# Optimization experiments

Measured on AMD Instinct MI355X. Metric: run time of the kernel, lower is better.

## Reference

```python
import jax, jax.numpy as jnp
import numpy as np

B, S, HID = 2, 2048, 2048
NK, NV, DK, DV, K = 16, 32, 128, 128, 4
KEY_DIM = NK * DK          # 2048
VAL_DIM = NV * DV          # 4096
CONV_DIM = 2 * KEY_DIM + VAL_DIM  # 8192
EPS = 1e-6


def setup_inputs() -> dict:
    key = jax.random.key(0)
    ks = jax.random.split(key, 8)
    n = lambda k, shape, sc: jax.random.normal(k, shape, jnp.float32) * sc
    return {
        "hidden_states": n(ks[0], (B, S, HID), 1.0),
        "W_qkv": n(ks[1], (CONV_DIM, HID), 0.02),
        "W_z": n(ks[2], (VAL_DIM, HID), 0.02),
        "W_b": n(ks[3], (NV, HID), 0.02),
        "W_a": n(ks[4], (NV, HID), 0.02),
        "conv_w": n(ks[5], (CONV_DIM, K), 0.3),   # depthwise conv weight, squeeze(1) of [C,1,K]
        "norm_w": jnp.ones((DV,), jnp.float32),
        "W_out": n(ks[6], (HID, VAL_DIM), 0.02),
        "dt_bias": jnp.ones((NV,), jnp.float32),
        "A_log": jnp.zeros((NV,), jnp.float32),
    }


def _l2norm(t):
    return t * jax.lax.rsqrt(jnp.sum(t * t, axis=-1, keepdims=True) + EPS)


def _forward(hidden_states, W_qkv, W_z, W_b, W_a, conv_w, norm_w, W_out, dt_bias, A_log):
    b_, s_, _ = hidden_states.shape
    mixed = hidden_states @ W_qkv.T                     # [B,S,CONV_DIM]
    z = (hidden_states @ W_z.T).reshape(b_, s_, NV, DV)  # gate branch
    b_proj = hidden_states @ W_b.T                      # [B,S,NV]
    a_proj = hidden_states @ W_a.T                      # [B,S,NV]

    # causal depthwise conv1d (groups=CONV_DIM, no bias) + silu
    x = jnp.transpose(mixed, (0, 2, 1))                 # [B,C,S]
    x = jnp.pad(x, ((0, 0), (0, 0), (K - 1, 0)))
    x = jax.lax.conv_general_dilated(
        x, conv_w[:, None, :], window_strides=(1,), padding="VALID",
        feature_group_count=CONV_DIM)
    mixed = jnp.transpose(jax.nn.silu(x), (0, 2, 1))    # [B,S,CONV_DIM]

    q, k, v = jnp.split(mixed, [KEY_DIM, 2 * KEY_DIM], axis=-1)
    q = q.reshape(b_, s_, NK, DK)
    k = k.reshape(b_, s_, NK, DK)
    v = v.reshape(b_, s_, NV, DV)

    beta = jax.nn.sigmoid(b_proj)                                    # [B,S,NV]
    g = -jnp.exp(A_log) * jax.nn.softplus(a_proj + dt_bias)          # [B,S,NV], log decay

    rep = NV // NK
    q = jnp.repeat(q, rep, axis=2)                      # GQA expand -> [B,S,NV,DK]
    k = jnp.repeat(k, rep, axis=2)
    q = _l2norm(q)
    k = _l2norm(k)
    scale = DK ** -0.5

    def step(state, inp):  # state: [B,NV,DK,DV]
        qt, kt, vt, gt, bt = inp  # [B,NV,DK],[B,NV,DK],[B,NV,DV],[B,NV],[B,NV]
        state = state * jnp.exp(gt)[..., None, None]
        mem = jnp.einsum('bhk,bhkv->bhv', kt, state)
        delta = (vt - mem) * bt[..., None]
        state = state + jnp.einsum('bhk,bhv->bhkv', kt, delta)
        ot = jnp.einsum('bhk,bhkv->bhv', qt * scale, state)
        return state, ot

    init = jnp.zeros((b_, NV, DK, DV), jnp.float32)
    xs = (jnp.moveaxis(q, 1, 0), jnp.moveaxis(k, 1, 0), jnp.moveaxis(v, 1, 0),
          jnp.moveaxis(g, 1, 0), jnp.moveaxis(beta, 1, 0))
    _, o = jax.lax.scan(step, init, xs)                 # [S,B,NV,DV]
    o = jnp.moveaxis(o, 0, 1)                           # [B,S,NV,DV]

    # RMSNormGated over head_v_dim, then silu(z) gate
    var = jnp.mean(o * o, axis=-1, keepdims=True)
    o = o * jax.lax.rsqrt(var + EPS) * norm_w
    o = (o * jax.nn.silu(z)).reshape(b_, s_, VAL_DIM)
    return o @ W_out.T


def reference(hidden_states, W_qkv, W_z, W_b, W_a, conv_w, norm_w, W_out, dt_bias, A_log):
    return _forward(hidden_states, W_qkv, W_z, W_b, W_a, conv_w, norm_w, W_out, dt_bias, A_log)
```

## Files before the change

### kernel.cpp

```cpp
#include <hip/hip_runtime.h>
#include <hip/hip_bf16.h>
#include <math.h>

#define DEVI __device__ __forceinline__

typedef __attribute__((ext_vector_type(4))) float f32x4;
typedef __attribute__((ext_vector_type(8))) short s16x8;
typedef __attribute__((ext_vector_type(4))) unsigned int u32x4;

DEVI float bf2f(ushort u){ union{unsigned int i; float f;} x; x.i = ((unsigned int)u)<<16; return x.f; }
DEVI ushort f2bf(float f){ union{float f; unsigned int i;} x; x.f = f;
  unsigned int r = x.i + 0x7fffu + ((x.i>>16)&1u); return (ushort)(r>>16); }

#define MFMA16(a,b,c) __builtin_amdgcn_mfma_f32_16x16x32_bf16(a,b,c,0,0,0)

__global__ __launch_bounds__(256) void cvt_bf16(const float* __restrict__ in, ushort* __restrict__ out){
  int i = blockIdx.x*256 + threadIdx.x;
  float4 v = ((const float4*)in)[i];
  ushort4 o; o.x = f2bf(v.x); o.y = f2bf(v.y); o.z = f2bf(v.z); o.w = f2bf(v.w);
  ((ushort4*)out)[i] = o;
}

DEVI void gl_lds16(const ushort* g, ushort* l){
  __builtin_amdgcn_global_load_lds((const __attribute__((address_space(1))) void*)g,
                                   (__attribute__((address_space(3))) void*)l, 16, 0, 0);
}

#define SBAR() __builtin_amdgcn_s_barrier()
#define LGKM0() do{ asm volatile("s_waitcnt lgkmcnt(0)" ::: "memory"); __builtin_amdgcn_sched_barrier(0); }while(0)
#define VMC6() asm volatile("s_waitcnt vmcnt(6)" ::: "memory")

template<int BF16_OUT>
__global__ __launch_bounds__(512, 2) void gemm256(const ushort* __restrict__ A,
                                                  const ushort* __restrict__ B,
                                                  void* __restrict__ Cv,
                                                  int M, int N, int K){
  __shared__ ushort smem[65536];
  __shared__ ushort dummy[4096];
  const int tid = threadIdx.x, w = tid>>6, lane = tid&63;
  const int fr = lane&15, quad = lane>>4;
  const int wm = w>>2, wn = w&3;
  const int NT = K>>6;

  const int nwg = gridDim.x, bid = blockIdx.x;
  const int wg = (bid&7)*(nwg>>3) + (bid>>3);
  const int nbn = N>>8;
  const long tileM = (long)(wg/nbn)<<8, tileN = (long)(wg%nbn)<<8;

  const int rr  = (tid&63)>>2;
  const int cc  = ((tid&3)*8) ^ ((rr&8)?16:0);
  const int row0 = (w>>1)*16 + rr;
  const int col0 = (w&1)*32 + cc;
  const long off0 = (long)row0*K + col0;
  const long h64 = 64l*K;

  const ushort* pA0 = A + tileM*K + off0;
  const ushort* pA1 = pA0 + 128l*K;
  const ushort* pB0 = B + tileN*K + off0;
  const ushort* pB1 = pB0 + 128l*K;

  const int dw = w*512;
  ushort* dmy = dummy + dw;

#define ST_A0(bb,tt) do{ if((tt)<NT){ const long kk=(long)(tt)<<6; \
    gl_lds16(pA0+kk, smem+(bb)*32768+dw);        gl_lds16(pA1+kk, smem+(bb)*32768+8192+dw);} \
    else { gl_lds16(pA0, dmy); gl_lds16(pA1, dmy);} }while(0)
#define ST_A1(bb,tt) do{ if((tt)<NT){ const long kk=((long)(tt)<<6)+h64; \
    gl_lds16(pA0+kk, smem+(bb)*32768+4096+dw);   gl_lds16(pA1+kk, smem+(bb)*32768+12288+dw);} \
    else { gl_lds16(pA0, dmy); gl_lds16(pA1, dmy);} }while(0)
#define ST_B0(bb,tt) do{ if((tt)<NT){ const long kk=(long)(tt)<<6; \
    gl_lds16(pB0+kk, smem+(bb)*32768+16384+dw);  gl_lds16(pB1+kk, smem+(bb)*32768+24576+dw);} \
    else { gl_lds16(pB0, dmy); gl_lds16(pB1, dmy);} }while(0)
#define ST_B1(bb,tt) do{ if((tt)<NT){ const long kk=((long)(tt)<<6)+h64; \
    gl_lds16(pB0+kk, smem+(bb)*32768+20480+dw);  gl_lds16(pB1+kk, smem+(bb)*32768+28672+dw);} \
    else { gl_lds16(pB0, dmy); gl_lds16(pB1, dmy);} }while(0)

  const int baseF = fr*32 + ((quad*8) ^ ((fr&8)?16:0));
  const int sB = (wn&1)*4;

  f32x4 acc[8][4];
  #pragma unroll
  for (int i=0;i<8;i++)
    #pragma unroll
    for (int j=0;j<4;j++) acc[i][j] = (f32x4){0.f,0.f,0.f,0.f};

  ST_A0(0,0); ST_B0(0,0); ST_B1(0,0); ST_A1(0,0);
  ST_A0(1,1); ST_B0(1,1); ST_B1(1,1);
  VMC6();
  SBAR();

  #pragma unroll 2
  for (int t=0; t<NT; ++t){
    const int bs = t&1;
    const ushort* SA = smem + bs*32768 + wm*8192;
    const ushort* SB = smem + bs*32768 + 16384 + (wn>>1)*8192;
    s16x8 af[4][2], bl[2][2], bh[2][2];
    #pragma unroll
    for (int mt=0;mt<4;mt++)
      #pragma unroll
      for (int ks=0;ks<2;ks++)
        af[mt][ks] = *(const s16x8*)(SA + ((mt*2+ks)<<9) + baseF);
    #pragma unroll
    for (int nt=0;nt<2;nt++)
      #pragma unroll
      for (int ks=0;ks<2;ks++)
        bl[nt][ks] = *(const s16x8*)(SB + (((sB+nt)*2+ks)<<9) + baseF);
    ST_A1(bs^1, t+1);
    SBAR(); LGKM0();
    __builtin_amdgcn_s_setprio(1);
    #pragma unroll
    for (int mt=0;mt<4;mt++)
      #pragma unroll
      for (int nt=0;nt<2;nt++){
        acc[mt][nt] = MFMA16(af[mt][0], bl[nt][0], acc[mt][nt]);
        acc[mt][nt] = MFMA16(af[mt][1], bl[nt][1], acc[mt][nt]);
      }
    __builtin_amdgcn_s_setprio(0);
    SBAR();
    #pragma unroll
    for (int nt=0;nt<2;nt++)
      #pragma unroll
      for (int ks=0;ks<2;ks++)
        bh[nt][ks] = *(const s16x8*)(SB + (((sB+2+nt)*2+ks)<<9) + baseF);
    ST_A0(bs, t+2);
    SBAR(); LGKM0();
    __builtin_amdgcn_s_setprio(1);
    #pragma unroll
    for (int mt=0;mt<4;mt++)
      #pragma unroll
      for (int nt=0;nt<2;nt++){
        acc[mt][2+nt] = MFMA16(af[mt][0], bh[nt][0], acc[mt][2+nt]);
        acc[mt][2+nt] = MFMA16(af[mt][1], bh[nt][1], acc[mt][2+nt]);
      }
    __builtin_amdgcn_s_setprio(0);
    SBAR();
    #pragma unroll
    for (int mt=0;mt<4;mt++)
      #pragma unroll
      for (int ks=0;ks<2;ks++)
        af[mt][ks] = *(const s16x8*)(SA + (((4+mt)*2+ks)<<9) + baseF);
    ST_B0(bs, t+2);
    SBAR(); LGKM0();
    __builtin_amdgcn_s_setprio(1);
    #pragma unroll
    for (int mt=0;mt<4;mt++)
      #pragma unroll
      for (int nt=0;nt<2;nt++){
        acc[4+mt][nt] = MFMA16(af[mt][0], bl[nt][0], acc[4+mt][nt]);
        acc[4+mt][nt] = MFMA16(af[mt][1], bl[nt][1], acc[4+mt][nt]);
      }
    __builtin_amdgcn_s_setprio(0);
    SBAR();
    ST_B1(bs, t+2);
    SBAR();
    __builtin_amdgcn_s_setprio(1);
    #pragma unroll
    for (int mt=0;mt<4;mt++)
      #pragma unroll
      for (int nt=0;nt<2;nt++){
        acc[4+mt][2+nt] = MFMA16(af[mt][0], bh[nt][0], acc[4+mt][2+nt]);
        acc[4+mt][2+nt] = MFMA16(af[mt][1], bh[nt][1], acc[4+mt][2+nt]);
      }
    __builtin_amdgcn_s_setprio(0);
    VMC6();
    SBAR();
  }
#undef ST_A0
#undef ST_A1
#undef ST_B0
#undef ST_B1

  const long Rb = tileM + wm*128 + quad*4;
  const long Cb = tileN + wn*64 + fr;
  if (BF16_OUT){
    ushort* C = (ushort*)Cv;
    #pragma unroll
    for (int mt=0;mt<8;mt++)
      #pragma unroll
      for (int r=0;r<4;r++){
        const long row = Rb + mt*16 + r;
        #pragma unroll
        for (int nt=0;nt<4;nt++)
          C[row*(long)N + Cb + nt*16] = f2bf(acc[mt][nt][r]);
      }
  } else {
    float* C = (float*)Cv;
    #pragma unroll
    for (int mt=0;mt<8;mt++)
      #pragma unroll
      for (int r=0;r<4;r++){
        const long row = Rb + mt*16 + r;
        #pragma unroll
        for (int nt=0;nt<4;nt++)
          C[row*(long)N + Cb + nt*16] = acc[mt][nt][r];
      }
  }
}

template<int BF16_OUT>
__global__ __launch_bounds__(256, 2) void gemm_bt(const ushort* __restrict__ A,
                                                  const ushort* __restrict__ B,
                                                  void* __restrict__ Cv,
                                                  int M, int N, int K){
  __shared__ ushort As[128*32];
  __shared__ ushort Bs[128*32];
  const int nb = N >> 7;
  const int tile_m = (blockIdx.x / nb) << 7;
  const int tile_n = (blockIdx.x % nb) << 7;
  const int tid  = threadIdx.x;
  const int w    = tid >> 6;
  const int lane = tid & 63;

  const int ca = w*2;
  const long rowA = tile_m + ca*16 + (lane>>2);
  const long rowB = tile_n + ca*16 + (lane>>2);
  const int  colE = (lane&3)*8;
  const ushort* pA0 = A + rowA*(long)K + colE;
  const ushort* pA1 = pA0 + 16l*K;
  const ushort* pB0 = B + rowB*(long)K + colE;
  const ushort* pB1 = pB0 + 16l*K;
  ushort* lA0 = As + ca*512;
  ushort* lA1 = As + ca*512 + 512;
  ushort* lB0 = Bs + ca*512;
  ushort* lB1 = Bs + ca*512 + 512;

  const int wr = (w>>1)<<6;
  const int wc = (w&1)<<6;
  const int fr = lane & 15;
  const int fk = (lane>>4)<<3;

  f32x4 acc[4][4];
  #pragma unroll
  for (int i=0;i<4;i++)
    #pragma unroll
    for (int j=0;j<4;j++) acc[i][j] = (f32x4){0.f,0.f,0.f,0.f};

  for (int k0 = 0; k0 < K; k0 += 32){
    __syncthreads();
    gl_lds16(pA0, lA0);
    gl_lds16(pA1, lA1);
    gl_lds16(pB0, lB0);
    gl_lds16(pB1, lB1);
    __syncthreads();
    s16x8 af[4], bfr[4];
    #pragma unroll
    for (int t=0;t<4;t++){
      af[t]  = *(const s16x8*)(As + (wr + t*16 + fr)*32 + fk);
      bfr[t] = *(const s16x8*)(Bs + (wc + t*16 + fr)*32 + fk);
    }
    #pragma unroll
    for (int mt=0;mt<4;mt++)
      #pragma unroll
      for (int nt=0;nt<4;nt++)
        acc[mt][nt] = MFMA16(af[mt], bfr[nt], acc[mt][nt]);
    pA0 += 32; pA1 += 32; pB0 += 32; pB1 += 32;
  }

  const int crow = tile_m + wr + ((lane>>4)<<2);
  const int ccol = tile_n + wc + (lane&15);
  if (BF16_OUT){
    ushort* C = (ushort*)Cv;
    #pragma unroll
    for (int mt=0;mt<4;mt++)
      #pragma unroll
      for (int r=0;r<4;r++){
        long row = crow + mt*16 + r;
        #pragma unroll
        for (int nt=0;nt<4;nt++)
          C[row*(long)N + ccol + nt*16] = f2bf(acc[mt][nt][r]);
      }
  } else {
    float* C = (float*)Cv;
    #pragma unroll
    for (int mt=0;mt<4;mt++)
      #pragma unroll
      for (int r=0;r<4;r++){
        long row = crow + mt*16 + r;
        #pragma unroll
        for (int nt=0;nt<4;nt++)
          C[row*(long)N + ccol + nt*16] = acc[mt][nt][r];
      }
  }
}

__global__ __launch_bounds__(256) void ba_post(const float* __restrict__ bapr,
    const float* __restrict__ dtb, const float* __restrict__ alog,
    float* __restrict__ beta, float* __restrict__ glog){
  const int idx = blockIdx.x*256 + threadIdx.x;
  const int m = idx >> 6, j = idx & 63;
  const float v = bapr[(long)m*128 + j];
  if (j < 32){
    beta[(long)m*32 + j] = 1.f/(1.f+expf(-v));
  } else {
    const int n = j - 32;
    float ap = v + dtb[n];
    float sp = (ap > 20.f) ? ap : log1pf(expf(ap));
    glog[(long)m*32 + n] = -expf(alog[n]) * sp;
  }
}

__global__ __launch_bounds__(256) void conv_qkv2(const ushort* __restrict__ mixed,
    const float* __restrict__ convw, ushort* __restrict__ qn, ushort* __restrict__ kn,
    ushort* __restrict__ vv){
  const long m0 = (long)blockIdx.x * 32;
  const int ct = blockIdx.y;
  const int ch = (ct<<11) + threadIdx.x*8;
  const ushort* base = mixed + ch;

  ushort* outp; int mode; float qsc = 1.f;
  if (ct == 0){ outp = qn + ch;        mode = 0; qsc = 0.08838834764831845f; }
  else if (ct == 1){ outp = kn + (ch-2048); mode = 1; }
  else { outp = vv + (ch-4096); mode = 2; }

  float cw0[8], cw1[8], cw2[8], cw3[8];
  #pragma unroll
  for (int e=0;e<8;e++){
    float4 wv = *(const float4*)(convw + (long)(ch+e)*4);
    cw0[e]=wv.x; cw1[e]=wv.y; cw2[e]=wv.z; cw3[e]=wv.w;
  }

#define LDROW(PTR, R) do{ s16x8 _v = *(const s16x8*)(PTR); \
    _Pragma("unroll") \
    for (int e=0;e<8;e++) R[e] = bf2f((ushort)_v[e]); }while(0)

#define STEP(P0,P1,P2,P3,MR) do{ \
    float y[8]; float ss = 0.f; \
    _Pragma("unroll") \
    for (int e=0;e<8;e++){ \
      float a = P0[e]*cw0[e]; \
      a += P1[e]*cw1[e]; \
      a += P2[e]*cw2[e]; \
      a += P3[e]*cw3[e]; \
      float sv = a / (1.f + expf(-a)); \
      y[e] = sv; ss += sv*sv; } \
    if (mode < 2){ \
      ss += __shfl_xor(ss,1); ss += __shfl_xor(ss,2); \
      ss += __shfl_xor(ss,4); ss += __shfl_xor(ss,8); \
      const float r_ = rsqrtf(ss + 1e-6f) * qsc; \
      s16x8 ov; \
      _Pragma("unroll") \
      for (int e=0;e<8;e++) ov[e] = (short)f2bf(y[e]*r_); \
      *(s16x8*)(outp + (MR)*2048) = ov; \
    } else { \
      s16x8 ov; \
      _Pragma("unroll") \
      for (int e=0;e<8;e++) ov[e] = (short)f2bf(y[e]); \
      *(s16x8*)(outp + (MR)*4096) = ov; \
    } \
  }while(0)

  float w3[8], w2[8], w1[8];
  if (((int)m0 & 2047) == 0){
    #pragma unroll
    for (int e=0;e<8;e++){ w3[e]=0.f; w2[e]=0.f; w1[e]=0.f; }
  } else {
    LDROW(base + (m0-3)*8192, w3);
    LDROW(base + (m0-2)*8192, w2);
    LDROW(base + (m0-1)*8192, w1);
  }

  long m = m0;
  for (int it=0; it<8; ++it){
    float r0[8], r1[8], r2[8], r3[8];
    LDROW(base + (m+0)*8192, r0);
    LDROW(base + (m+1)*8192, r1);
    LDROW(base + (m+2)*8192, r2);
    LDROW(base + (m+3)*8192, r3);
    STEP(w3,w2,w1,r0, m+0);
    STEP(w2,w1,r0,r1, m+1);
    STEP(w1,r0,r1,r2, m+2);
    STEP(r0,r1,r2,r3, m+3);
    #pragma unroll
    for (int e=0;e<8;e++){ w3[e]=r1[e]; w2[e]=r2[e]; w1[e]=r3[e]; }
    m += 4;
  }
#undef LDROW
#undef STEP
}

__global__ __launch_bounds__(256) void chunk_prep(
    const ushort* __restrict__ qn, const ushort* __restrict__ kn,
    const float* __restrict__ beta, const float* __restrict__ glog,
    ushort* __restrict__ Tg, ushort* __restrict__ Mg, float* __restrict__ cumLgG){
  const int bid = blockIdx.x;
  const int bh = bid >> 6, ch = bid & 63;
  const int b = bh>>5, h = bh&31, hq = h>>1;
  const long tch = (long)b*2048 + ch*32;
  const int tid = threadIdx.x, w = tid>>6, lane = tid&63;
  const int quad = lane>>4, l15 = lane&15;

  __shared__ __attribute__((aligned(16))) ushort Kl[32][136];
  __shared__ __attribute__((aligned(16))) ushort Ql[32][136];
  __shared__ float Asl[32][33];
  __shared__ float Lgl[32], Btl[32];

  const int sc = tid>>3, ss = (tid&7)*16;
  {
    const ushort* kp = kn + (tch+sc)*2048 + hq*128 + ss;
    const ushort* qp = qn + (tch+sc)*2048 + hq*128 + ss;
    *(u32x4*)&Kl[sc][ss] = *(const u32x4*)kp; *(u32x4*)&Kl[sc][ss+8] = *(const u32x4*)(kp+8);
    *(u32x4*)&Ql[sc][ss] = *(const u32x4*)qp; *(u32x4*)&Ql[sc][ss+8] = *(const u32x4*)(qp+8);
  }
  if (tid < 64){
    const int c = lane & 31;
    float gv = glog[(tch + c)*32 + h];
    float bv = beta[(tch + c)*32 + h];
    #pragma unroll
    for (int off=1; off<32; off<<=1){
      float t = __shfl_up(gv, off);
      if ((lane & 31) >= off) gv += t;
    }
    if (lane < 32){ Lgl[c] = gv; Btl[c] = bv; cumLgG[(long)bid*32 + c] = gv; }
  }
  __syncthreads();

  const int mt = w>>1, nt = w&1;
  s16x8 ka[4], qa[4], kb[4];
  #pragma unroll
  for (int ks=0; ks<4; ks++){
    ka[ks] = *(const s16x8*)&Kl[mt*16+l15][ks*32 + quad*8];
    qa[ks] = *(const s16x8*)&Ql[mt*16+l15][ks*32 + quad*8];
    kb[ks] = *(const s16x8*)&Kl[nt*16+l15][ks*32 + quad*8];
  }
  f32x4 accK = (f32x4){0.f,0.f,0.f,0.f}, accQ = (f32x4){0.f,0.f,0.f,0.f};
  #pragma unroll
  for (int ks=0; ks<4; ks++){
    accK = MFMA16(ka[ks], kb[ks], accK);
    accQ = MFMA16(qa[ks], kb[ks], accQ);
  }
  const int j = nt*16 + l15;
  const float Lgj = Lgl[j];
  #pragma unroll
  for (int i=0;i<4;i++){
    const int r = mt*16 + quad*4 + i;
    const float e = expf(Lgl[r]-Lgj);
    Asl[r][j] = (r>j) ? -Btl[r]*e*accK[i] : 0.f;
    Mg[(long)bid*1024 + r*32 + j] = (r>=j) ? f2bf(e*accQ[i]) : (ushort)0;
  }
  __syncthreads();

  if (tid < 32){
    const int jc = tid;
    float tc[32];
    #pragma unroll
    for (int c=0;c<32;c++){
      float acc = (c==jc) ? 1.f : 0.f;
      #pragma unroll
      for (int i2=0;i2<c;i2++) acc = fmaf(Asl[c][i2], tc[i2], acc);
      tc[c] = acc;
      Tg[(long)bid*1024 + c*32 + jc] = f2bf(acc);
    }
  }
}

__global__ __launch_bounds__(256, 2) void chunk_scan3(
    const ushort* __restrict__ qn, const ushort* __restrict__ kn,
    const ushort* __restrict__ vv, const float* __restrict__ beta,
    const float* __restrict__ cumLg, const ushort* __restrict__ Tg,
    const ushort* __restrict__ Mg, float* __restrict__ o){
  const int bh = blockIdx.x & 63, sl = blockIdx.x >> 6;
  const int b = bh>>5, h = bh&31, hq = h>>1;
  const int dv0 = sl<<4;
  const int tid = threadIdx.x, w = tid>>6, lane = tid&63;
  const int quad = lane>>4, l15 = lane&15;
  const int rt = w&1, kq = w>>1;

  __shared__ __attribute__((aligned(16))) ushort STl[16][136];
  __shared__ __attribute__((aligned(16))) ushort B0T[16][40];
  __shared__ __attribute__((aligned(16))) ushort DT[16][40];
  __shared__ float Btf[32], eLgl[32], eDf[32];

  const ushort* pKQ = (kq ? qn : kn) + ((long)b*2048 + rt*16 + l15)*2048 + hq*128 + quad*8;
  const ushort* pKT = kn + ((long)b*2048 + quad*8)*2048 + hq*128 + w*32 + l15;
  const ushort* pV  = vv + ((long)b*2048 + rt*16 + quad*4)*4096 + h*128 + dv0 + l15;
  const ushort* pTM = (kq ? Mg : Tg) + (long)bh*65536 + (rt*16 + l15)*32 + quad*8;
  const long pbBase = (long)bh*2048 + tid;
  const float* betaP = beta + ((long)b*2048 + tid)*32 + h;

  s16x8 cKQ[4], nKQ[4], cK0, cK1, nK0, nK1, cTM, nTM;
  ushort cV0=0,cV1=0,cV2=0,cV3=0, nV0=0,nV1=0,nV2=0,nV3=0;
  float cLg = 0.f, nLg = 0.f, cBt = 0.f, nBt = 0.f;

  f32x4 S0 = (f32x4){0.f,0.f,0.f,0.f}, S1 = (f32x4){0.f,0.f,0.f,0.f};

#define LOADCH(PKQ,PK0,PK1,PV0,PV1,PV2,PV3,PTMv,PLG,PBT,CH) do{ \
    const long co = (long)(CH)*65536; \
    _Pragma("unroll") \
    for (int ks=0; ks<4; ks++) PKQ[ks] = *(const s16x8*)(pKQ + co + ks*32); \
    _Pragma("unroll") \
    for (int e=0; e<8; e++){ \
      PK0[e] = (short)pKT[co + (long)e*2048]; \
      PK1[e] = (short)pKT[co + (long)e*2048 + 16]; } \
    if (kq == 0){ \
      const long vo = (long)(CH)*131072; \
      PV0 = pV[vo]; PV1 = pV[vo+4096]; PV2 = pV[vo+8192]; PV3 = pV[vo+12288]; } \
    PTMv = *(const s16x8*)(pTM + (long)(CH)*1024); \
    if (tid < 32){ PLG = cumLg[pbBase + (long)(CH)*32]; PBT = betaP[(long)(CH)*1024]; } \
  }while(0)

  LOADCH(cKQ, cK0, cK1, cV0,cV1,cV2,cV3, cTM, cLg, cBt, 0);

  for (int ch=0; ch<64; ch++){
    const long tch = (long)b*2048 + ch*32;
    LOADCH(nKQ, nK0, nK1, nV0,nV1,nV2,nV3, nTM, nLg, nBt, (ch<63)?(ch+1):63);
    if (tid < 32){
      float lgC = __shfl(cLg, 31);
      Btf[tid] = cBt;
      eLgl[tid] = expf(cLg);
      eDf[tid]  = expf(lgC - cLg);
    }
    {
      ushort4 p0, p1;
      p0.x=f2bf(S0[0]); p0.y=f2bf(S0[1]); p0.z=f2bf(S0[2]); p0.w=f2bf(S0[3]);
      p1.x=f2bf(S1[0]); p1.y=f2bf(S1[1]); p1.z=f2bf(S1[2]); p1.w=f2bf(S1[3]);
      *(ushort4*)&STl[l15][w*32 + quad*4]      = p0;
      *(ushort4*)&STl[l15][w*32 + 16 + quad*4] = p1;
    }
    __syncthreads();
    f32x4 acc = (f32x4){0.f,0.f,0.f,0.f};
    #pragma unroll
    for (int ks=0; ks<4; ks++){
      s16x8 sb = *(const s16x8*)&STl[l15][ks*32 + quad*8];
      acc = MFMA16(cKQ[ks], sb, acc);
    }
    if (kq == 0){
      const int c0r = rt*16 + quad*4;
      ushort4 pb;
      pb.x = f2bf(Btf[c0r+0]*(bf2f(cV0) - eLgl[c0r+0]*acc[0]));
      pb.y = f2bf(Btf[c0r+1]*(bf2f(cV1) - eLgl[c0r+1]*acc[1]));
      pb.z = f2bf(Btf[c0r+2]*(bf2f(cV2) - eLgl[c0r+2]*acc[2]));
      pb.w = f2bf(Btf[c0r+3]*(bf2f(cV3) - eLgl[c0r+3]*acc[3]));
      *(ushort4*)&B0T[l15][rt*16 + quad*4] = pb;
    } else {
      #pragma unroll
      for (int i=0;i<4;i++) acc[i] *= eLgl[rt*16 + quad*4 + i];
    }
    __syncthreads();
    const float eC = eLgl[31];
    s16x8 kta0, kta1;
    #pragma unroll
    for (int e=0;e<8;e++){
      const float ed = eDf[quad*8 + e];
      kta0[e] = (short)f2bf(bf2f((ushort)cK0[e])*ed);
      kta1[e] = (short)f2bf(bf2f((ushort)cK1[e])*ed);
    }
    if (kq == 0){
      s16x8 a = *(const s16x8*)&B0T[l15][quad*8];
      f32x4 Dt = MFMA16(a, cTM, ((f32x4){0.f,0.f,0.f,0.f}));
      #pragma unroll
      for (int i=0;i<4;i++)
        DT[quad*4+i][rt*16 + l15] = f2bf(Dt[i]);
    }
    __syncthreads();
    s16x8 df = *(const s16x8*)&DT[l15][quad*8];
    if (kq == 1){
      f32x4 O = MFMA16(cTM, df, acc);
      #pragma unroll
      for (int i=0;i<4;i++)
        o[(tch + rt*16 + quad*4 + i)*4096 + h*128 + dv0 + l15] = O[i];
    }
    f32x4 t0, t1;
    #pragma unroll
    for (int i=0;i<4;i++){ t0[i] = S0[i]*eC; t1[i] = S1[i]*eC; }
    S0 = MFMA16(kta0, df, t0);
    S1 = MFMA16(kta1, df, t1);
    #pragma unroll
    for (int ks=0; ks<4; ks++) cKQ[ks] = nKQ[ks];
    cK0 = nK0; cK1 = nK1; cTM = nTM;
    cV0 = nV0; cV1 = nV1; cV2 = nV2; cV3 = nV3;
    cLg = nLg; cBt = nBt;
  }
#undef LOADCH
}

__global__ __launch_bounds__(128) void norm_gate(const float* __restrict__ o,
    const ushort* __restrict__ z, const float* __restrict__ normw,
    ushort* __restrict__ og){
  const long mh = blockIdx.x;
  const int d = threadIdx.x;
  float x = o[mh*128 + d];
  float ss = x*x;
  #pragma unroll
  for (int off=32; off; off>>=1) ss += __shfl_xor(ss, off);
  __shared__ float w2[2];
  if ((d&63)==0) w2[d>>6] = ss;
  __syncthreads();
  float r = rsqrtf((w2[0]+w2[1])*(1.f/128.f) + 1e-6f);
  float zz = bf2f(z[mh*128 + d]);
  float sil = zz / (1.f + expf(-zz));
  og[mh*128 + d] = f2bf(x*r*normw[d]*sil);
}

extern "C" void kernel_launch(void* const* d_in, const int* in_sizes, int n_in,
                              void* d_out, int out_size, void* d_ws, size_t ws_size,
                              hipStream_t stream){
  const float* hs    = (const float*)d_in[0];
  const float* Wqkv  = (const float*)d_in[1];
  const float* Wz    = (const float*)d_in[2];
  const float* Wb    = (const float*)d_in[3];
  const float* Wa    = (const float*)d_in[4];
  const float* convw = (const float*)d_in[5];
  const float* normw = (const float*)d_in[6];
  const float* Wout  = (const float*)d_in[7];
  const float* dtb   = (const float*)d_in[8];
  const float* alog  = (const float*)d_in[9];

  char* ws = (char*)d_ws;
  ushort* hsb   = (ushort*)(ws);
  ushort* wqb   = (ushort*)(ws + (16l<<20));
  ushort* wzb   = (ushort*)(ws + (48l<<20));
  ushort* wob   = (ushort*)(ws + (64l<<20));
  ushort* mixed = (ushort*)(ws + (80l<<20));
  ushort* zb    = (ushort*)(ws + (144l<<20));
  float*  beta  = (float*)(ws + (176l<<20));
  float*  cumLg = (float*)(ws + (176l<<20) + (512l<<10));
  float*  glog  = (float*)(ws + (177l<<20));
  ushort* Tg    = (ushort*)(ws + (178l<<20));
  ushort* Mg    = (ushort*)(ws + (186l<<20));
  ushort* wbab  = (ushort*)(ws + (194l<<20));
  float*  bapr  = (float*)(ws + (195l<<20));
  ushort* kn = hsb;  ushort* qn = wzb;  ushort* vvp = wqb;  ushort* og = wqb;
  float*  o_raw = (float*)mixed;

  cvt_bf16<<<8192,  256, 0, stream>>>(hs,   hsb);
  cvt_bf16<<<16384, 256, 0, stream>>>(Wqkv, wqb);
  cvt_bf16<<<8192,  256, 0, stream>>>(Wz,   wzb);
  cvt_bf16<<<8192,  256, 0, stream>>>(Wout, wob);
  cvt_bf16<<<64,    256, 0, stream>>>(Wb,   wbab);
  cvt_bf16<<<64,    256, 0, stream>>>(Wa,   wbab + 65536);

  gemm256<1><<<512, 512, 0, stream>>>(hsb, wqb, (void*)mixed, 4096, 8192, 2048);
  gemm256<1><<<256, 512, 0, stream>>>(hsb, wzb, (void*)zb,    4096, 4096, 2048);
  gemm_bt<0><<<32*1,  256, 0, stream>>>(hsb, wbab, (void*)bapr, 4096, 128,  2048);
  ba_post<<<1024, 256, 0, stream>>>(bapr, dtb, alog, beta, glog);

  conv_qkv2<<<dim3(128,4), 256, 0, stream>>>(mixed, convw, qn, kn, vvp);
  chunk_prep<<<4096, 256, 0, stream>>>(qn, kn, beta, glog, Tg, Mg, cumLg);
  chunk_scan3<<<512, 256, 0, stream>>>(qn, kn, vvp, beta, cumLg, Tg, Mg, o_raw);
  norm_gate<<<131072, 128, 0, stream>>>(o_raw, zb, normw, og);

  gemm_bt<0><<<32*16, 256, 0, stream>>>(og, wob, d_out, 4096, 2048, 4096);
}
```

Measured before the change: 719.2 us.

## Add XCD-grouped tile mapping and 256x128 pipelined GEMM for output projection

Replaces the gemm256 workgroup-to-tile mapping with a grouping where each XCD handles a contiguous block of row and column tiles, to improve L2 reuse of A and B panels. Adds a new 256x128-tile GEMM variant with the same async global-to-LDS double-buffered MFMA pipeline. It is used for the output projection in place of the simpler 128x128 gemm_bt kernel. The grouping parameters are hard-coded per launch and must divide the tile counts exactly.

```diff
diff --git a/kernel.cpp b/kernel.cpp
--- a/kernel.cpp
+++ b/kernel.cpp
@@ -29,12 +29,14 @@
 #define SBAR() __builtin_amdgcn_s_barrier()
 #define LGKM0() do{ asm volatile("s_waitcnt lgkmcnt(0)" ::: "memory"); __builtin_amdgcn_sched_barrier(0); }while(0)
 #define VMC6() asm volatile("s_waitcnt vmcnt(6)" ::: "memory")
+#define VMC4() asm volatile("s_waitcnt vmcnt(4)" ::: "memory")
 
 template<int BF16_OUT>
 __global__ __launch_bounds__(512, 2) void gemm256(const ushort* __restrict__ A,
                                                   const ushort* __restrict__ B,
                                                   void* __restrict__ Cv,
-                                                  int M, int N, int K){
+                                                  int M, int N, int K,
+                                                  int rpx, int cpx){
   __shared__ ushort smem[65536];
   __shared__ ushort dummy[4096];
   const int tid = threadIdx.x, w = tid>>6, lane = tid&63;
@@ -42,10 +44,14 @@
   const int wm = w>>2, wn = w&3;
   const int NT = K>>6;
 
-  const int nwg = gridDim.x, bid = blockIdx.x;
-  const int wg = (bid&7)*(nwg>>3) + (bid>>3);
   const int nbn = N>>8;
-  const long tileM = (long)(wg/nbn)<<8, tileN = (long)(wg%nbn)<<8;
+  const int bid = blockIdx.x;
+  const int xcd = bid & 7, idx = bid >> 3;
+  const int CGn = nbn / cpx;
+  const int rgrp = xcd / CGn, cgrp = xcd % CGn;
+  const int rloc = idx % rpx, cloc = idx / rpx;
+  const long tileM = (long)(rgrp*rpx + rloc) << 8;
+  const long tileN = (long)(cgrp*cpx + cloc) << 8;
 
   const int rr  = (tid&63)>>2;
   const int cc  = ((tid&3)*8) ^ ((rr&8)?16:0);
@@ -192,6 +198,158 @@
         const long row = Rb + mt*16 + r;
         #pragma unroll
         for (int nt=0;nt<4;nt++)
+          C[row*(long)N + Cb + nt*16] = acc[mt][nt][r];
+      }
+  }
+}
+
+template<int BF16_OUT>
+__global__ __launch_bounds__(512, 2) void gemm256n128(const ushort* __restrict__ A,
+                                                      const ushort* __restrict__ B,
+                                                      void* __restrict__ Cv,
+                                                      int M, int N, int K,
+                                                      int rpx, int cpx){
+  __shared__ ushort smem[49152];
+  __shared__ ushort dummy[4096];
+  const int tid = threadIdx.x, w = tid>>6, lane = tid&63;
+  const int fr = lane&15, quad = lane>>4;
+  const int wm = w>>2, wn = w&3;
+  const int NT = K>>6;
+
+  const int nbn = N>>7;
+  const int bid = blockIdx.x;
+  const int xcd = bid & 7, idx = bid >> 3;
+  const int CGn = nbn / cpx;
+  const int rgrp = xcd / CGn, cgrp = xcd % CGn;
+  const int rloc = idx % rpx, cloc = idx / rpx;
+  const long tileM = (long)(rgrp*rpx + rloc) << 8;
+  const long tileN = (long)(cgrp*cpx + cloc) << 7;
+
+  const int rr  = (tid&63)>>2;
+  const int cc  = ((tid&3)*8) ^ ((rr&8)?16:0);
+  const int row0 = (w>>1)*16 + rr;
+  const int col0 = (w&1)*32 + cc;
+  const long off0 = (long)row0*K + col0;
+  const long h64 = 64l*K;
+
+  const ushort* pA0 = A + tileM*K + off0;
+  const ushort* pA1 = pA0 + 128l*K;
+  const ushort* pB0 = B + tileN*K + off0;
+
+  const int dw = w*512;
+  ushort* dmy = dummy + dw;
+
+#define ST_A0(bb,tt) do{ if((tt)<NT){ const long kk=(long)(tt)<<6; \
+    gl_lds16(pA0+kk, smem+(bb)*24576+dw);        gl_lds16(pA1+kk, smem+(bb)*24576+8192+dw);} \
+    else { gl_lds16(pA0, dmy); gl_lds16(pA1, dmy);} }while(0)
+#define ST_A1(bb,tt) do{ if((tt)<NT){ const long kk=((long)(tt)<<6)+h64; \
+    gl_lds16(pA0+kk, smem+(bb)*24576+4096+dw);   gl_lds16(pA1+kk, smem+(bb)*24576+12288+dw);} \
+    else { gl_lds16(pA0, dmy); gl_lds16(pA1, dmy);} }while(0)
+#define ST_B(bb,tt) do{ if((tt)<NT){ const long kk=(long)(tt)<<6; \
+    gl_lds16(pB0+kk, smem+(bb)*24576+16384+dw);  gl_lds16(pB0+kk+h64, smem+(bb)*24576+20480+dw);} \
+    else { gl_lds16(pB0, dmy); gl_lds16(pB0, dmy);} }while(0)
+
+  const int baseF = fr*32 + ((quad*8) ^ ((fr&8)?16:0));
+
+  f32x4 acc[8][2];
+  #pragma unroll
+  for (int i=0;i<8;i++)
+    #pragma unroll
+    for (int j=0;j<2;j++) acc[i][j] = (f32x4){0.f,0.f,0.f,0.f};
+
+  ST_A0(0,0); ST_B(0,0); ST_A1(0,0);
+  ST_A0(1,1); ST_B(1,1);
+  VMC4();
+  SBAR();
+
+  #pragma unroll 2
+  for (int t=0; t<NT; ++t){
+    const int bs = t&1;
+    const ushort* SA = smem + bs*24576 + wm*8192;
+    const ushort* SB = smem + bs*24576 + 16384;
+    s16x8 af[4][2], bl[2], bh[2];
+    #pragma unroll
+    for (int mt=0;mt<4;mt++)
+      #pragma unroll
+      for (int ks=0;ks<2;ks++)
+        af[mt][ks] = *(const s16x8*)(SA + ((mt*2+ks)<<9) + baseF);
+    #pragma unroll
+    for (int ks=0;ks<2;ks++)
+      bl[ks] = *(const s16x8*)(SB + (((wn*2+0)*2+ks)<<9) + baseF);
+    ST_A1(bs^1, t+1);
+    SBAR(); LGKM0();
+    __builtin_amdgcn_s_setprio(1);
+    #pragma unroll
+    for (int mt=0;mt<4;mt++){
+      acc[mt][0] = MFMA16(af[mt][0], bl[0], acc[mt][0]);
+      acc[mt][0] = MFMA16(af[mt][1], bl[1], acc[mt][0]);
+    }
+    __builtin_amdgcn_s_setprio(0);
+    SBAR();
+    #pragma unroll
+    for (int ks=0;ks<2;ks++)
+      bh[ks] = *(const s16x8*)(SB + (((wn*2+1)*2+ks)<<9) + baseF);
+    ST_A0(bs, t+2);
+    SBAR(); LGKM0();
+    __builtin_amdgcn_s_setprio(1);
+    #pragma unroll
+    for (int mt=0;mt<4;mt++){
+      acc[mt][1] = MFMA16(af[mt][0], bh[0], acc[mt][1]);
+      acc[mt][1] = MFMA16(af[mt][1], bh[1], acc[mt][1]);
+    }
+    __builtin_amdgcn_s_setprio(0);
+    SBAR();
+    #pragma unroll
+    for (int mt=0;mt<4;mt++)
+      #pragma unroll
+      for (int ks=0;ks<2;ks++)
+        af[mt][ks] = *(const s16x8*)(SA + (((4+mt)*2+ks)<<9) + baseF);
+    ST_B(bs, t+2);
+    SBAR(); LGKM0();
+    __builtin_amdgcn_s_setprio(1);
+    #pragma unroll
+    for (int mt=0;mt<4;mt++){
+      acc[4+mt][0] = MFMA16(af[mt][0], bl[0], acc[4+mt][0]);
+      acc[4+mt][0] = MFMA16(af[mt][1], bl[1], acc[4+mt][0]);
+    }
+    __builtin_amdgcn_s_setprio(0);
+    SBAR();
+    __builtin_amdgcn_s_setprio(1);
+    #pragma unroll
+    for (int mt=0;mt<4;mt++){
+      acc[4+mt][1] = MFMA16(af[mt][0], bh[0], acc[4+mt][1]);
+      acc[4+mt][1] = MFMA16(af[mt][1], bh[1], acc[4+mt][1]);
+    }
+    __builtin_amdgcn_s_setprio(0);
+    VMC4();
+    SBAR();
+  }
+#undef ST_A0
+#undef ST_A1
+#undef ST_B
+
+  const long Rb = tileM + wm*128 + quad*4;
+  const long Cb = tileN + wn*32 + fr;
+  if (BF16_OUT){
+    ushort* C = (ushort*)Cv;
+    #pragma unroll
+    for (int mt=0;mt<8;mt++)
+      #pragma unroll
+      for (int r=0;r<4;r++){
+        const long row = Rb + mt*16 + r;
+        #pragma unroll
+        for (int nt=0;nt<2;nt++)
+          C[row*(long)N + Cb + nt*16] = f2bf(acc[mt][nt][r]);
+      }
+  } else {
+    float* C = (float*)Cv;
+    #pragma unroll
+    for (int mt=0;mt<8;mt++)
+      #pragma unroll
+      for (int r=0;r<4;r++){
+        const long row = Rb + mt*16 + r;
+        #pragma unroll
+        for (int nt=0;nt<2;nt++)
           C[row*(long)N + Cb + nt*16] = acc[mt][nt][r];
       }
   }
@@ -629,8 +787,8 @@
   cvt_bf16<<<64,    256, 0, stream>>>(Wb,   wbab);
   cvt_bf16<<<64,    256, 0, stream>>>(Wa,   wbab + 65536);
 
-  gemm256<1><<<512, 512, 0, stream>>>(hsb, wqb, (void*)mixed, 4096, 8192, 2048);
-  gemm256<1><<<256, 512, 0, stream>>>(hsb, wzb, (void*)zb,    4096, 4096, 2048);
+  gemm256<1><<<512, 512, 0, stream>>>(hsb, wqb, (void*)mixed, 4096, 8192, 2048, 4, 16);
+  gemm256<1><<<256, 512, 0, stream>>>(hsb, wzb, (void*)zb,    4096, 4096, 2048, 4, 8);
   gemm_bt<0><<<32*1,  256, 0, stream>>>(hsb, wbab, (void*)bapr, 4096, 128,  2048);
   ba_post<<<1024, 256, 0, stream>>>(bapr, dtb, alog, beta, glog);
 
@@ -639,5 +797,5 @@
   chunk_scan3<<<512, 256, 0, stream>>>(qn, kn, vvp, beta, cumLg, Tg, Mg, o_raw);
   norm_gate<<<131072, 128, 0, stream>>>(o_raw, zb, normw, og);
 
-  gemm_bt<0><<<32*16, 256, 0, stream>>>(og, wob, d_out, 4096, 2048, 4096);
-}
+  gemm256n128<0><<<256, 512, 0, stream>>>(og, wob, d_out, 4096, 2048, 4096, 4, 8);
+}
```

Result: faster. 697.8 us (-3.0%).
